# Kernel tuning notes

Hardware: AMD Instinct MI355X
Metric: run time of the kernel (lower is better)

Reference implementation:

```python
import jax, jax.numpy as jnp
import numpy as np

D_MODEL = 1024
NUM_HEADS = 16
HEAD_DIM = D_MODEL // NUM_HEADS
WINDOW = 64
BATCH = 2
SEQ = 2048


def setup_inputs() -> dict:
    key = jax.random.key(0)
    ks = jax.random.split(key, 5)
    s = 1.0 / np.sqrt(D_MODEL)  # torch Linear-ish init scale
    x = jax.random.normal(ks[0], (BATCH, SEQ, D_MODEL), dtype=jnp.float32)
    Wq = jax.random.normal(ks[1], (D_MODEL, D_MODEL), dtype=jnp.float32) * s
    Wk = jax.random.normal(ks[2], (D_MODEL, D_MODEL), dtype=jnp.float32) * s
    Wv = jax.random.normal(ks[3], (D_MODEL, D_MODEL), dtype=jnp.float32) * s
    Wo = jax.random.normal(ks[4], (D_MODEL, D_MODEL), dtype=jnp.float32) * s
    z = jnp.zeros((D_MODEL,), dtype=jnp.float32)
    return {"x": x, "Wq": Wq, "bq": z, "Wk": Wk, "bk": z, "Wv": Wv, "bv": z,
            "Wo": Wo, "bo": z}


def reference(x, Wq, bq, Wk, bk, Wv, bv, Wo, bo):
    B, S, D = x.shape
    H, Hd = NUM_HEADS, HEAD_DIM
    # QKV projections; weights stored as [in, out] so y = x @ W + b
    q = (x @ Wq + bq).reshape(B, S, H, Hd).transpose(0, 2, 1, 3)  # bhsd
    k = (x @ Wk + bk).reshape(B, S, H, Hd).transpose(0, 2, 1, 3)
    v = (x @ Wv + bv).reshape(B, S, H, Hd).transpose(0, 2, 1, 3)
    scores = jnp.einsum('bhqd,bhkd->bhqk', q, k) / jnp.sqrt(jnp.float32(Hd))
    # static local-window band mask: attend only where |i - j| <= window_size
    idx = jnp.arange(S)
    dist = jnp.abs(idx[None, :] - idx[:, None])  # [S, S]
    scores = jnp.where(dist[None, None] > WINDOW, -jnp.inf, scores)
    attn = jax.nn.softmax(scores, axis=-1)
    out = jnp.einsum('bhqk,bhkd->bhqd', attn, v)
    out = out.transpose(0, 2, 1, 3).reshape(B, S, D)
    return out @ Wo + bo
```

## Files before the change

kernel.cpp:

```cpp
#include <hip/hip_runtime.h>
#include <cstdint>
#include <cstddef>

typedef __bf16 bf16x8 __attribute__((ext_vector_type(8)));
typedef float  f32x4  __attribute__((ext_vector_type(4)));

__device__ __forceinline__ unsigned short f2bf(float f) {
    union { __bf16 b; unsigned short u; } cv; cv.b = (__bf16)f; return cv.u;
}
__device__ __forceinline__ int iclamp(int v, int lo, int hi) {
    return v < lo ? lo : (v > hi ? hi : v);
}

__device__ __forceinline__ void gload16(const void* gsrc, void* ldsdst) {
    __builtin_amdgcn_global_load_lds(
        (const __attribute__((address_space(1))) unsigned int*)(uintptr_t)gsrc,
        (__attribute__((address_space(3))) unsigned int*)(uintptr_t)ldsdst,
        16, 0, 0);
}

#define MFMA16(a, b, c) __builtin_amdgcn_mfma_f32_16x16x32_bf16((a), (b), (c), 0, 0, 0)

__global__ __launch_bounds__(256) void castx(const float* __restrict__ x,
                                             unsigned short* __restrict__ xb) {
    size_t i = ((size_t)blockIdx.x * 256 + threadIdx.x) * 8;
    float4 a = *(const float4*)(x + i);
    float4 b = *(const float4*)(x + i + 4);
    union { unsigned short u[8]; uint4 q; } pk;
    pk.u[0] = f2bf(a.x); pk.u[1] = f2bf(a.y); pk.u[2] = f2bf(a.z); pk.u[3] = f2bf(a.w);
    pk.u[4] = f2bf(b.x); pk.u[5] = f2bf(b.y); pk.u[6] = f2bf(b.z); pk.u[7] = f2bf(b.w);
    *(uint4*)(xb + i) = pk.q;
}

__global__ __launch_bounds__(256) void wt_kernel(const float* __restrict__ Wq,
                                                 const float* __restrict__ Wk,
                                                 const float* __restrict__ Wv,
                                                 const float* __restrict__ Wo,
                                                 unsigned short* __restrict__ Wt) {
    __shared__ float tile[64][65];
    const int z = blockIdx.z;
    const float* W = (z == 0) ? Wq : (z == 1) ? Wk : (z == 2) ? Wv : Wo;
    const int n0 = blockIdx.x * 64, k0 = blockIdx.y * 64;
    const int tid = threadIdx.x;
    const int tr = tid >> 4, tc = (tid & 15) * 4;
#pragma unroll
    for (int i = 0; i < 4; ++i) {
        int r = tr + i * 16;
        float4 v = *(const float4*)(W + (size_t)(k0 + r) * 1024 + n0 + tc);
        tile[r][tc + 0] = v.x; tile[r][tc + 1] = v.y;
        tile[r][tc + 2] = v.z; tile[r][tc + 3] = v.w;
    }
    __syncthreads();
    const int n = tid & 63, kc = (tid >> 6) * 16;
    union { unsigned short u[16]; uint4 q[2]; } pk;
#pragma unroll
    for (int c = 0; c < 16; ++c) pk.u[c] = f2bf(tile[kc + c][n]);
    uint4* dst = (uint4*)(Wt + (size_t)z * 1048576 + (size_t)(n0 + n) * 1024 + k0 + kc);
    dst[0] = pk.q[0]; dst[1] = pk.q[1];
}

__global__ __launch_bounds__(256) void bias_cat_k(const float* __restrict__ bq,
                                                  const float* __restrict__ bk,
                                                  const float* __restrict__ bv,
                                                  float* __restrict__ bc) {
    int i = blockIdx.x * 256 + threadIdx.x;
    bc[i] = (i < 1024) ? bq[i] : (i < 2048) ? bk[i - 1024] : bv[i - 2048];
}

__device__ __forceinline__ void gemm_mainloop(const unsigned short* __restrict__ A,
                                              const unsigned short* __restrict__ Bt,
                                              int K, int m0, int n0,
                                              unsigned short* Asm, unsigned short* Bsm,
                                              f32x4 acc[4][4]) {
    const int tid = threadIdx.x;
    const int wave = tid >> 6, lane = tid & 63;
    const int lq = lane & 15, quad = lane >> 4;

    const int rstage = wave * 16 + (lane >> 2);
    const int sw8 = ((lane & 3) ^ quad) * 8;
    const unsigned short* gA0 = A + (size_t)(m0 + rstage) * K + sw8;
    const unsigned short* gA1 = A + (size_t)(m0 + 64 + rstage) * K + sw8;
    const unsigned short* gB0 = Bt + (size_t)(n0 + rstage) * K + sw8;
    const unsigned short* gB1 = Bt + (size_t)(n0 + 64 + rstage) * K + sw8;
    unsigned short* lA0 = Asm + (wave * 16) * 32;
    unsigned short* lA1 = Asm + (64 + wave * 16) * 32;
    unsigned short* lB0 = Bsm + (wave * 16) * 32;
    unsigned short* lB1 = Bsm + (64 + wave * 16) * 32;

    int offA[4], offB[4];
    const int pos8 = (quad ^ (lq >> 2)) * 8;
#pragma unroll
    for (int i = 0; i < 4; ++i) {
        offA[i] = ((wave >> 1) * 64 + i * 16 + lq) * 32 + pos8;
        offB[i] = ((wave & 1) * 64 + i * 16 + lq) * 32 + pos8;
    }

    for (int kt = 0; kt < K; kt += 32) {
        gload16(gA0 + kt, lA0);
        gload16(gA1 + kt, lA1);
        gload16(gB0 + kt, lB0);
        gload16(gB1 + kt, lB1);
        __syncthreads();
        bf16x8 af[4], bfr[4];
#pragma unroll
        for (int i = 0; i < 4; ++i) af[i] = *(const bf16x8*)(Asm + offA[i]);
#pragma unroll
        for (int j = 0; j < 4; ++j) bfr[j] = *(const bf16x8*)(Bsm + offB[j]);
#pragma unroll
        for (int i = 0; i < 4; ++i)
#pragma unroll
            for (int j = 0; j < 4; ++j)
                acc[i][j] = MFMA16(af[i], bfr[j], acc[i][j]);
        __syncthreads();
    }
}

__global__ __launch_bounds__(256, 2) void gemm_qkv(const unsigned short* __restrict__ xb,
                                                   const unsigned short* __restrict__ Wt,
                                                   const float* __restrict__ bcat,
                                                   unsigned short* __restrict__ Qb,
                                                   unsigned short* __restrict__ Kb,
                                                   unsigned short* __restrict__ Vt) {
    __shared__ __align__(16) unsigned short smem[8192];
    unsigned short* Asm = smem;
    unsigned short* Bsm = smem + 4096;
    f32x4 acc[4][4];
#pragma unroll
    for (int i = 0; i < 4; ++i)
#pragma unroll
        for (int j = 0; j < 4; ++j) acc[i][j] = f32x4{0.f, 0.f, 0.f, 0.f};
    const int m0 = blockIdx.y * 128, n0 = blockIdx.x * 128;
    gemm_mainloop(xb, Wt, 1024, m0, n0, Asm, Bsm, acc);

    const int tid = threadIdx.x, wave = tid >> 6, lane = tid & 63;
    const int lq = lane & 15, quad = lane >> 4;
    const int p = n0 >> 10;
    const int nloc = (wave & 1) * 64;
    const int c64 = (n0 + nloc) & 1023;
    const int h = c64 >> 6;
    const int b = m0 >> 11;
    const int mw = m0 + (wave >> 1) * 64;
    const int mloc = mw & 2047;
    unsigned short* sw = smem + wave * 1152;

    float bi[4];
#pragma unroll
    for (int j = 0; j < 4; ++j) bi[j] = bcat[n0 + nloc + j * 16 + lq];

    unsigned short* qkbase = (p == 0) ? Qb : Kb;

#pragma unroll
    for (int i = 0; i < 4; ++i) {
#pragma unroll
        for (int j = 0; j < 4; ++j)
#pragma unroll
            for (int r = 0; r < 4; ++r)
                sw[(quad * 4 + r) * 72 + j * 16 + lq] = f2bf(acc[i][j][r] + bi[j]);
        if (p < 2) {
            const int row = lane >> 2, c0 = (lane & 3) * 8;
            uint4 v0 = *(const uint4*)(sw + row * 72 + c0);
            uint4 v1 = *(const uint4*)(sw + row * 72 + c0 + 32);
            const int s = mloc + i * 16 + row;
            unsigned short* dp = qkbase + ((size_t)((b * 16 + h) * 2048 + s)) * 64;
            *(uint4*)(dp + c0) = v0;
            *(uint4*)(dp + c0 + 32) = v1;
        } else {
#pragma unroll
            for (int th = 0; th < 2; ++th) {
                union { unsigned short u[8]; uint4 q; } pk;
#pragma unroll
                for (int t = 0; t < 8; ++t) pk.u[t] = sw[(th * 8 + t) * 72 + lane];
                const int sbase = mloc + i * 16 + th * 8;
                *(uint4*)(Vt + ((size_t)((b * 16 + h) * 64 + lane)) * 2048 + sbase) = pk.q;
            }
        }
    }
}

__global__ __launch_bounds__(256, 4) void attn_k(const unsigned short* __restrict__ Qb,
                                                 const unsigned short* __restrict__ Kb,
                                                 const unsigned short* __restrict__ Vt,
                                                 unsigned short* __restrict__ AO) {
    __shared__ __align__(16) unsigned short P[4][16 * 168];
    const int tid = threadIdx.x, wave = tid >> 6, lane = tid & 63;
    const int lq = lane & 15, quad = lane >> 4;
    const int b = blockIdx.z, h = blockIdx.y;
    const int q0 = blockIdx.x * 64 + wave * 16;
    const unsigned short* Qh = Qb + (size_t)((b * 16 + h) * 2048) * 64;
    const unsigned short* Kh = Kb + (size_t)((b * 16 + h) * 2048) * 64;
    const unsigned short* Vh = Vt + (size_t)((b * 16 + h) * 64) * 2048;
    unsigned short* pw = P[wave];

    {
        unsigned int* zp = (unsigned int*)(pw + (lane >> 2) * 168 + 144 + (lane & 3) * 4);
        zp[0] = 0u; zp[1] = 0u;
    }

    const bf16x8 qa0 = *(const bf16x8*)(Qh + (size_t)(q0 + lq) * 64 + quad * 8);
    const bf16x8 qa1 = *(const bf16x8*)(Qh + (size_t)(q0 + lq) * 64 + 32 + quad * 8);

    float sc[9][4];
    float mr[4] = {-3e38f, -3e38f, -3e38f, -3e38f};
#pragma unroll
    for (int t = 0; t < 9; ++t) {
        const int kb = q0 - 64 + t * 16;
        const int krow = kb + lq;
        const int krc = iclamp(krow, 0, 2047);
        const unsigned short* kp = Kh + (size_t)krc * 64 + quad * 8;
        const bf16x8 kf0 = *(const bf16x8*)kp;
        const bf16x8 kf1 = *(const bf16x8*)(kp + 32);
        f32x4 cacc = f32x4{0.f, 0.f, 0.f, 0.f};
        cacc = MFMA16(qa0, kf0, cacc);
        cacc = MFMA16(qa1, kf1, cacc);
#pragma unroll
        for (int r = 0; r < 4; ++r) {
            const int q = q0 + quad * 4 + r;
            const int dj = q - krow;
            const bool ok = (krow >= 0) && (krow < 2048) && (dj <= 64) && (dj >= -64);
            const float s = ok ? cacc[r] * 0.125f : -3e38f;
            sc[t][r] = s;
            mr[r] = fmaxf(mr[r], s);
        }
    }
#pragma unroll
    for (int r = 0; r < 4; ++r) {
#pragma unroll
        for (int off = 1; off < 16; off <<= 1)
            mr[r] = fmaxf(mr[r], __shfl_xor(mr[r], off));
    }
    float ls[4] = {0.f, 0.f, 0.f, 0.f};
#pragma unroll
    for (int t = 0; t < 9; ++t)
#pragma unroll
        for (int r = 0; r < 4; ++r) {
            const float p = __expf(sc[t][r] - mr[r]);
            sc[t][r] = p;
            ls[r] += p;
        }
#pragma unroll
    for (int r = 0; r < 4; ++r) {
#pragma unroll
        for (int off = 1; off < 16; off <<= 1)
            ls[r] += __shfl_xor(ls[r], off);
    }
    float rinv[4];
#pragma unroll
    for (int r = 0; r < 4; ++r) rinv[r] = 1.f / ls[r];

#pragma unroll
    for (int t = 0; t < 9; ++t)
#pragma unroll
        for (int r = 0; r < 4; ++r)
            pw[(quad * 4 + r) * 168 + t * 16 + lq] = f2bf(sc[t][r]);

    f32x4 oa[4];
#pragma unroll
    for (int dt = 0; dt < 4; ++dt) oa[dt] = f32x4{0.f, 0.f, 0.f, 0.f};
#pragma unroll
    for (int ks = 0; ks < 5; ++ks) {
        const bf16x8 pf = *(const bf16x8*)(pw + lq * 168 + ks * 32 + quad * 8);
        int s0 = q0 - 64 + ks * 32 + quad * 8;
        s0 = iclamp(s0, 0, 2040);
#pragma unroll
        for (int dt = 0; dt < 4; ++dt) {
            const bf16x8 vf = *(const bf16x8*)(Vh + (size_t)(dt * 16 + lq) * 2048 + s0);
            oa[dt] = MFMA16(pf, vf, oa[dt]);
        }
    }
#pragma unroll
    for (int dt = 0; dt < 4; ++dt)
#pragma unroll
        for (int r = 0; r < 4; ++r) {
            const int q = q0 + quad * 4 + r;
            AO[(size_t)(b * 2048 + q) * 1024 + h * 64 + dt * 16 + lq] =
                f2bf(oa[dt][r] * rinv[r]);
        }
}

__global__ __launch_bounds__(256, 2) void gemm_out(const unsigned short* __restrict__ AO,
                                                   const unsigned short* __restrict__ Wot,
                                                   const float* __restrict__ bo,
                                                   float* __restrict__ out) {
    __shared__ __align__(16) unsigned short Asm[128 * 32];
    __shared__ __align__(16) unsigned short Bsm[64 * 32];
    const int tid = threadIdx.x, wave = tid >> 6, lane = tid & 63;
    const int lq = lane & 15, quad = lane >> 4;
    const int m0 = blockIdx.y * 128, n0 = blockIdx.x * 64;

    f32x4 acc[4][2];
#pragma unroll
    for (int i = 0; i < 4; ++i)
#pragma unroll
        for (int j = 0; j < 2; ++j) acc[i][j] = f32x4{0.f, 0.f, 0.f, 0.f};

    const int rstage = wave * 16 + (lane >> 2);
    const int sw8 = ((lane & 3) ^ quad) * 8;
    const unsigned short* gA0 = AO + (size_t)(m0 + rstage) * 1024 + sw8;
    const unsigned short* gA1 = AO + (size_t)(m0 + 64 + rstage) * 1024 + sw8;
    const unsigned short* gB0 = Wot + (size_t)(n0 + rstage) * 1024 + sw8;
    unsigned short* lA0 = Asm + (wave * 16) * 32;
    unsigned short* lA1 = Asm + (64 + wave * 16) * 32;
    unsigned short* lB0 = Bsm + (wave * 16) * 32;

    int offA[4], offB[2];
    const int pos8 = (quad ^ (lq >> 2)) * 8;
#pragma unroll
    for (int i = 0; i < 4; ++i)
        offA[i] = ((wave >> 1) * 64 + i * 16 + lq) * 32 + pos8;
#pragma unroll
    for (int j = 0; j < 2; ++j)
        offB[j] = ((wave & 1) * 32 + j * 16 + lq) * 32 + pos8;

    for (int kt = 0; kt < 1024; kt += 32) {
        gload16(gA0 + kt, lA0);
        gload16(gA1 + kt, lA1);
        gload16(gB0 + kt, lB0);
        __syncthreads();
        bf16x8 af[4], bfr[2];
#pragma unroll
        for (int i = 0; i < 4; ++i) af[i] = *(const bf16x8*)(Asm + offA[i]);
#pragma unroll
        for (int j = 0; j < 2; ++j) bfr[j] = *(const bf16x8*)(Bsm + offB[j]);
#pragma unroll
        for (int i = 0; i < 4; ++i)
#pragma unroll
            for (int j = 0; j < 2; ++j)
                acc[i][j] = MFMA16(af[i], bfr[j], acc[i][j]);
        __syncthreads();
    }

#pragma unroll
    for (int i = 0; i < 4; ++i) {
#pragma unroll
        for (int j = 0; j < 2; ++j) {
            const int n = n0 + (wave & 1) * 32 + j * 16 + lq;
            const float bi = bo[n];
#pragma unroll
            for (int r = 0; r < 4; ++r) {
                const int m = m0 + (wave >> 1) * 64 + i * 16 + quad * 4 + r;
                out[(size_t)m * 1024 + n] = acc[i][j][r] + bi;
            }
        }
    }
}

extern "C" void kernel_launch(void* const* d_in, const int* in_sizes, int n_in,
                              void* d_out, int out_size, void* d_ws, size_t ws_size,
                              hipStream_t stream) {
    const float* x  = (const float*)d_in[0];
    const float* Wq = (const float*)d_in[1];
    const float* bq = (const float*)d_in[2];
    const float* Wk = (const float*)d_in[3];
    const float* bk = (const float*)d_in[4];
    const float* Wv = (const float*)d_in[5];
    const float* bv = (const float*)d_in[6];
    const float* Wo = (const float*)d_in[7];
    const float* bo = (const float*)d_in[8];
    float* out = (float*)d_out;

    unsigned short* us = (unsigned short*)d_ws;
    const size_t MEG = 1048576;
    unsigned short* xb = us;
    unsigned short* Wt = us + 4 * MEG;
    unsigned short* Qb = us + 8 * MEG;
    unsigned short* Kb = us + 12 * MEG;
    unsigned short* Vt = us + 16 * MEG;
    unsigned short* AO = us + 20 * MEG;
    float* bcat = (float*)(us + 24 * MEG);

    castx<<<2048, 256, 0, stream>>>(x, xb);
    wt_kernel<<<dim3(16, 16, 4), 256, 0, stream>>>(Wq, Wk, Wv, Wo, Wt);
    bias_cat_k<<<12, 256, 0, stream>>>(bq, bk, bv, bcat);
    gemm_qkv<<<dim3(24, 32), 256, 0, stream>>>(xb, Wt, bcat, Qb, Kb, Vt);
    attn_k<<<dim3(32, 16, 2), 256, 0, stream>>>(Qb, Kb, Vt, AO);
    gemm_out<<<dim3(16, 32), 256, 0, stream>>>(AO, Wt + 3 * MEG, bo, out);
}
```

Measured before the change: 174.4 us.

## Fuse prep kernels, deepen QKV GEMM K-tile, skip interior masks, coalesce attention stores

Merges the x cast, weight transpose and bias concat into one launch to cut launch overhead. The QKV GEMM now stages 64-wide K tiles with an 8-way XOR swizzle and runs two MFMA sub-steps per barrier pair, which halves the number of barriers, and its launch-bounds occupancy hint goes from 2 to 3. The attention kernel skips band and bounds masking on interior key tiles and in non-edge blocks. It also stages its output through LDS so each row is written with 16-byte stores. The larger LDS footprint (32KB) may limit occupancy, and the pw buffer is reused for output without a barrier, relying on per-wave ownership.

```diff
diff --git a/kernel.cpp b/kernel.cpp
--- a/kernel.cpp
+++ b/kernel.cpp
@@ -21,119 +21,118 @@
 
 #define MFMA16(a, b, c) __builtin_amdgcn_mfma_f32_16x16x32_bf16((a), (b), (c), 0, 0, 0)
 
-__global__ __launch_bounds__(256) void castx(const float* __restrict__ x,
-                                             unsigned short* __restrict__ xb) {
-    size_t i = ((size_t)blockIdx.x * 256 + threadIdx.x) * 8;
-    float4 a = *(const float4*)(x + i);
-    float4 b = *(const float4*)(x + i + 4);
-    union { unsigned short u[8]; uint4 q; } pk;
-    pk.u[0] = f2bf(a.x); pk.u[1] = f2bf(a.y); pk.u[2] = f2bf(a.z); pk.u[3] = f2bf(a.w);
-    pk.u[4] = f2bf(b.x); pk.u[5] = f2bf(b.y); pk.u[6] = f2bf(b.z); pk.u[7] = f2bf(b.w);
-    *(uint4*)(xb + i) = pk.q;
-}
-
-__global__ __launch_bounds__(256) void wt_kernel(const float* __restrict__ Wq,
-                                                 const float* __restrict__ Wk,
-                                                 const float* __restrict__ Wv,
-                                                 const float* __restrict__ Wo,
-                                                 unsigned short* __restrict__ Wt) {
+__global__ __launch_bounds__(256) void prep_k(const float* __restrict__ x,
+                                              const float* __restrict__ Wq,
+                                              const float* __restrict__ Wk,
+                                              const float* __restrict__ Wv,
+                                              const float* __restrict__ Wo,
+                                              const float* __restrict__ bq,
+                                              const float* __restrict__ bk,
+                                              const float* __restrict__ bv,
+                                              unsigned short* __restrict__ xb,
+                                              unsigned short* __restrict__ Wt,
+                                              float* __restrict__ bc) {
     __shared__ float tile[64][65];
-    const int z = blockIdx.z;
-    const float* W = (z == 0) ? Wq : (z == 1) ? Wk : (z == 2) ? Wv : Wo;
-    const int n0 = blockIdx.x * 64, k0 = blockIdx.y * 64;
-    const int tid = threadIdx.x;
-    const int tr = tid >> 4, tc = (tid & 15) * 4;
-#pragma unroll
-    for (int i = 0; i < 4; ++i) {
-        int r = tr + i * 16;
-        float4 v = *(const float4*)(W + (size_t)(k0 + r) * 1024 + n0 + tc);
-        tile[r][tc + 0] = v.x; tile[r][tc + 1] = v.y;
-        tile[r][tc + 2] = v.z; tile[r][tc + 3] = v.w;
-    }
-    __syncthreads();
-    const int n = tid & 63, kc = (tid >> 6) * 16;
-    union { unsigned short u[16]; uint4 q[2]; } pk;
-#pragma unroll
-    for (int c = 0; c < 16; ++c) pk.u[c] = f2bf(tile[kc + c][n]);
-    uint4* dst = (uint4*)(Wt + (size_t)z * 1048576 + (size_t)(n0 + n) * 1024 + k0 + kc);
-    dst[0] = pk.q[0]; dst[1] = pk.q[1];
-}
-
-__global__ __launch_bounds__(256) void bias_cat_k(const float* __restrict__ bq,
-                                                  const float* __restrict__ bk,
-                                                  const float* __restrict__ bv,
-                                                  float* __restrict__ bc) {
-    int i = blockIdx.x * 256 + threadIdx.x;
-    bc[i] = (i < 1024) ? bq[i] : (i < 2048) ? bk[i - 1024] : bv[i - 2048];
-}
-
-__device__ __forceinline__ void gemm_mainloop(const unsigned short* __restrict__ A,
-                                              const unsigned short* __restrict__ Bt,
-                                              int K, int m0, int n0,
-                                              unsigned short* Asm, unsigned short* Bsm,
-                                              f32x4 acc[4][4]) {
-    const int tid = threadIdx.x;
-    const int wave = tid >> 6, lane = tid & 63;
-    const int lq = lane & 15, quad = lane >> 4;
-
-    const int rstage = wave * 16 + (lane >> 2);
-    const int sw8 = ((lane & 3) ^ quad) * 8;
-    const unsigned short* gA0 = A + (size_t)(m0 + rstage) * K + sw8;
-    const unsigned short* gA1 = A + (size_t)(m0 + 64 + rstage) * K + sw8;
-    const unsigned short* gB0 = Bt + (size_t)(n0 + rstage) * K + sw8;
-    const unsigned short* gB1 = Bt + (size_t)(n0 + 64 + rstage) * K + sw8;
-    unsigned short* lA0 = Asm + (wave * 16) * 32;
-    unsigned short* lA1 = Asm + (64 + wave * 16) * 32;
-    unsigned short* lB0 = Bsm + (wave * 16) * 32;
-    unsigned short* lB1 = Bsm + (64 + wave * 16) * 32;
-
-    int offA[4], offB[4];
-    const int pos8 = (quad ^ (lq >> 2)) * 8;
-#pragma unroll
-    for (int i = 0; i < 4; ++i) {
-        offA[i] = ((wave >> 1) * 64 + i * 16 + lq) * 32 + pos8;
-        offB[i] = ((wave & 1) * 64 + i * 16 + lq) * 32 + pos8;
-    }
-
-    for (int kt = 0; kt < K; kt += 32) {
-        gload16(gA0 + kt, lA0);
-        gload16(gA1 + kt, lA1);
-        gload16(gB0 + kt, lB0);
-        gload16(gB1 + kt, lB1);
-        __syncthreads();
-        bf16x8 af[4], bfr[4];
-#pragma unroll
-        for (int i = 0; i < 4; ++i) af[i] = *(const bf16x8*)(Asm + offA[i]);
-#pragma unroll
-        for (int j = 0; j < 4; ++j) bfr[j] = *(const bf16x8*)(Bsm + offB[j]);
-#pragma unroll
-        for (int i = 0; i < 4; ++i)
-#pragma unroll
-            for (int j = 0; j < 4; ++j)
-                acc[i][j] = MFMA16(af[i], bfr[j], acc[i][j]);
-        __syncthreads();
-    }
-}
-
-__global__ __launch_bounds__(256, 2) void gemm_qkv(const unsigned short* __restrict__ xb,
+    const int bx = blockIdx.x, tid = threadIdx.x;
+    if (bx < 1024) {
+        const int z = bx >> 8, t = bx & 255;
+        const float* W = (z == 0) ? Wq : (z == 1) ? Wk : (z == 2) ? Wv : Wo;
+        const int n0 = (t & 15) * 64, k0 = (t >> 4) * 64;
+        const int tr = tid >> 4, tc = (tid & 15) * 4;
+#pragma unroll
+        for (int i = 0; i < 4; ++i) {
+            int r = tr + i * 16;
+            float4 v = *(const float4*)(W + (size_t)(k0 + r) * 1024 + n0 + tc);
+            tile[r][tc + 0] = v.x; tile[r][tc + 1] = v.y;
+            tile[r][tc + 2] = v.z; tile[r][tc + 3] = v.w;
+        }
+        __syncthreads();
+        const int n = tid & 63, kc = (tid >> 6) * 16;
+        union { unsigned short u[16]; uint4 q[2]; } pk;
+#pragma unroll
+        for (int c = 0; c < 16; ++c) pk.u[c] = f2bf(tile[kc + c][n]);
+        uint4* dst = (uint4*)(Wt + (size_t)z * 1048576 + (size_t)(n0 + n) * 1024 + k0 + kc);
+        dst[0] = pk.q[0]; dst[1] = pk.q[1];
+    } else if (bx < 3072) {
+        size_t i = ((size_t)(bx - 1024) * 256 + tid) * 8;
+        float4 a = *(const float4*)(x + i);
+        float4 b = *(const float4*)(x + i + 4);
+        union { unsigned short u[8]; uint4 q; } pk;
+        pk.u[0] = f2bf(a.x); pk.u[1] = f2bf(a.y); pk.u[2] = f2bf(a.z); pk.u[3] = f2bf(a.w);
+        pk.u[4] = f2bf(b.x); pk.u[5] = f2bf(b.y); pk.u[6] = f2bf(b.z); pk.u[7] = f2bf(b.w);
+        *(uint4*)(xb + i) = pk.q;
+    } else {
+        int i = (bx - 3072) * 256 + tid;
+        bc[i] = (i < 1024) ? bq[i] : (i < 2048) ? bk[i - 1024] : bv[i - 2048];
+    }
+}
+
+__global__ __launch_bounds__(256, 3) void gemm_qkv(const unsigned short* __restrict__ xb,
                                                    const unsigned short* __restrict__ Wt,
                                                    const float* __restrict__ bcat,
                                                    unsigned short* __restrict__ Qb,
                                                    unsigned short* __restrict__ Kb,
                                                    unsigned short* __restrict__ Vt) {
-    __shared__ __align__(16) unsigned short smem[8192];
-    unsigned short* Asm = smem;
-    unsigned short* Bsm = smem + 4096;
-    f32x4 acc[4][4];
-#pragma unroll
-    for (int i = 0; i < 4; ++i)
-#pragma unroll
-        for (int j = 0; j < 4; ++j) acc[i][j] = f32x4{0.f, 0.f, 0.f, 0.f};
-    const int m0 = blockIdx.y * 128, n0 = blockIdx.x * 128;
-    gemm_mainloop(xb, Wt, 1024, m0, n0, Asm, Bsm, acc);
-
+    __shared__ __align__(16) unsigned short Asm[128 * 64];
+    __shared__ __align__(16) unsigned short Bsm[128 * 64];
     const int tid = threadIdx.x, wave = tid >> 6, lane = tid & 63;
     const int lq = lane & 15, quad = lane >> 4;
+    const int m0 = blockIdx.y * 128, n0 = blockIdx.x * 128;
+
+    f32x4 acc[4][4];
+#pragma unroll
+    for (int i = 0; i < 4; ++i)
+#pragma unroll
+        for (int j = 0; j < 4; ++j) acc[i][j] = f32x4{0.f, 0.f, 0.f, 0.f};
+
+    const int r8 = lane >> 3, cs = lane & 7;
+    const int gch = (cs ^ r8) * 8;
+    const unsigned short* gA[4];
+    const unsigned short* gB[4];
+    unsigned short* lA[4];
+    unsigned short* lB[4];
+#pragma unroll
+    for (int s = 0; s < 4; ++s) {
+        const int r = wave * 32 + s * 8 + r8;
+        gA[s] = xb + (size_t)(m0 + r) * 1024 + gch;
+        gB[s] = Wt + (size_t)(n0 + r) * 1024 + gch;
+        lA[s] = Asm + (wave * 32 + s * 8) * 64;
+        lB[s] = Bsm + (wave * 32 + s * 8) * 64;
+    }
+
+    int offA[4][2], offB[4][2];
+#pragma unroll
+    for (int i = 0; i < 4; ++i)
+#pragma unroll
+        for (int kk = 0; kk < 2; ++kk) {
+            const int rA = (wave >> 1) * 64 + i * 16 + lq;
+            const int rB = (wave & 1) * 64 + i * 16 + lq;
+            offA[i][kk] = rA * 64 + (((kk * 4 + quad) ^ (lq & 7)) * 8);
+            offB[i][kk] = rB * 64 + (((kk * 4 + quad) ^ (lq & 7)) * 8);
+        }
+
+    for (int kt = 0; kt < 1024; kt += 64) {
+#pragma unroll
+        for (int s = 0; s < 4; ++s) gload16(gA[s] + kt, lA[s]);
+#pragma unroll
+        for (int s = 0; s < 4; ++s) gload16(gB[s] + kt, lB[s]);
+        __syncthreads();
+#pragma unroll
+        for (int kk = 0; kk < 2; ++kk) {
+            bf16x8 af[4], bfr[4];
+#pragma unroll
+            for (int i = 0; i < 4; ++i) af[i] = *(const bf16x8*)(Asm + offA[i][kk]);
+#pragma unroll
+            for (int j = 0; j < 4; ++j) bfr[j] = *(const bf16x8*)(Bsm + offB[j][kk]);
+#pragma unroll
+            for (int i = 0; i < 4; ++i)
+#pragma unroll
+                for (int j = 0; j < 4; ++j)
+                    acc[i][j] = MFMA16(af[i], bfr[j], acc[i][j]);
+        }
+        __syncthreads();
+    }
+
     const int p = n0 >> 10;
     const int nloc = (wave & 1) * 64;
     const int c64 = (n0 + nloc) & 1023;
@@ -141,7 +140,7 @@
     const int b = m0 >> 11;
     const int mw = m0 + (wave >> 1) * 64;
     const int mloc = mw & 2047;
-    unsigned short* sw = smem + wave * 1152;
+    unsigned short* sw = Asm + wave * 1152;
 
     float bi[4];
 #pragma unroll
@@ -186,6 +185,7 @@
     const int lq = lane & 15, quad = lane >> 4;
     const int b = blockIdx.z, h = blockIdx.y;
     const int q0 = blockIdx.x * 64 + wave * 16;
+    const bool edge = (blockIdx.x == 0) || (blockIdx.x == 31);
     const unsigned short* Qh = Qb + (size_t)((b * 16 + h) * 2048) * 64;
     const unsigned short* Kh = Kb + (size_t)((b * 16 + h) * 2048) * 64;
     const unsigned short* Vh = Vt + (size_t)((b * 16 + h) * 64) * 2048;
@@ -203,23 +203,32 @@
     float mr[4] = {-3e38f, -3e38f, -3e38f, -3e38f};
 #pragma unroll
     for (int t = 0; t < 9; ++t) {
-        const int kb = q0 - 64 + t * 16;
-        const int krow = kb + lq;
-        const int krc = iclamp(krow, 0, 2047);
+        const int krow = q0 - 64 + t * 16 + lq;
+        const bool need_mask = (t == 0) || (t == 8) || edge;
+        const int krc = need_mask ? iclamp(krow, 0, 2047) : krow;
         const unsigned short* kp = Kh + (size_t)krc * 64 + quad * 8;
         const bf16x8 kf0 = *(const bf16x8*)kp;
         const bf16x8 kf1 = *(const bf16x8*)(kp + 32);
         f32x4 cacc = f32x4{0.f, 0.f, 0.f, 0.f};
         cacc = MFMA16(qa0, kf0, cacc);
         cacc = MFMA16(qa1, kf1, cacc);
-#pragma unroll
-        for (int r = 0; r < 4; ++r) {
-            const int q = q0 + quad * 4 + r;
-            const int dj = q - krow;
-            const bool ok = (krow >= 0) && (krow < 2048) && (dj <= 64) && (dj >= -64);
-            const float s = ok ? cacc[r] * 0.125f : -3e38f;
-            sc[t][r] = s;
-            mr[r] = fmaxf(mr[r], s);
+        if (need_mask) {
+#pragma unroll
+            for (int r = 0; r < 4; ++r) {
+                const int q = q0 + quad * 4 + r;
+                const int dj = q - krow;
+                const bool ok = (krow >= 0) && (krow < 2048) && (dj <= 64) && (dj >= -64);
+                const float s = ok ? cacc[r] * 0.125f : -3e38f;
+                sc[t][r] = s;
+                mr[r] = fmaxf(mr[r], s);
+            }
+        } else {
+#pragma unroll
+            for (int r = 0; r < 4; ++r) {
+                const float s = cacc[r] * 0.125f;
+                sc[t][r] = s;
+                mr[r] = fmaxf(mr[r], s);
+            }
         }
     }
 #pragma unroll
@@ -267,14 +276,20 @@
             oa[dt] = MFMA16(pf, vf, oa[dt]);
         }
     }
+
 #pragma unroll
     for (int dt = 0; dt < 4; ++dt)
 #pragma unroll
-        for (int r = 0; r < 4; ++r) {
-            const int q = q0 + quad * 4 + r;
-            AO[(size_t)(b * 2048 + q) * 1024 + h * 64 + dt * 16 + lq] =
-                f2bf(oa[dt][r] * rinv[r]);
-        }
+        for (int r = 0; r < 4; ++r)
+            pw[(quad * 4 + r) * 72 + dt * 16 + lq] = f2bf(oa[dt][r] * rinv[r]);
+    {
+        const int row = lane >> 2, c0 = (lane & 3) * 16;
+        uint4 v0 = *(const uint4*)(pw + row * 72 + c0);
+        uint4 v1 = *(const uint4*)(pw + row * 72 + c0 + 8);
+        unsigned short* dp = AO + (size_t)(b * 2048 + q0 + row) * 1024 + h * 64 + c0;
+        *(uint4*)(dp) = v0;
+        *(uint4*)(dp + 8) = v1;
+    }
 }
 
 __global__ __launch_bounds__(256, 2) void gemm_out(const unsigned short* __restrict__ AO,
@@ -368,9 +383,7 @@
     unsigned short* AO = us + 20 * MEG;
     float* bcat = (float*)(us + 24 * MEG);
 
-    castx<<<2048, 256, 0, stream>>>(x, xb);
-    wt_kernel<<<dim3(16, 16, 4), 256, 0, stream>>>(Wq, Wk, Wv, Wo, Wt);
-    bias_cat_k<<<12, 256, 0, stream>>>(bq, bk, bv, bcat);
+    prep_k<<<3084, 256, 0, stream>>>(x, Wq, Wk, Wv, Wo, bq, bk, bv, xb, Wt, bcat);
     gemm_qkv<<<dim3(24, 32), 256, 0, stream>>>(xb, Wt, bcat, Qb, Kb, Vt);
     attn_k<<<dim3(32, 16, 2), 256, 0, stream>>>(Qb, Kb, Vt, AO);
     gemm_out<<<dim3(16, 32), 256, 0, stream>>>(AO, Wt + 3 * MEG, bo, out);
```

Result: faster. 164.4 us (-5.7%).
